# Kernel tuning notes

Measured on AMD Instinct MI355X. Metric: run time of the kernel, lower is better.

The kernel has to match this reference:

```python
import jax, jax.numpy as jnp
import numpy as np

N = 8192          # nodes
E = 131072        # edges (avg degree 16)
F_IN = 4          # in_channels
F_HID = 128       # GCNConv output channels (hard-coded in module)
C = 16            # out_channels = number of clusters
EPS = 1e-15


def setup_inputs() -> dict:
    key = jax.random.key(0)
    ks = jax.random.split(key, 6)
    x = jax.random.normal(ks[0], (N, F_IN), dtype=jnp.float32)
    W1 = jax.random.normal(ks[1], (F_IN, F_HID), dtype=jnp.float32) / np.sqrt(F_IN)
    b1 = jax.random.normal(ks[2], (F_HID,), dtype=jnp.float32) * 0.01
    Wp = jax.random.normal(ks[3], (F_HID, C), dtype=jnp.float32) / np.sqrt(F_HID)
    bp = jax.random.normal(ks[4], (C,), dtype=jnp.float32) * 0.01
    edge_index = jax.random.randint(ks[5], (2, E), 0, N, dtype=jnp.int64)
    batch = jnp.zeros((N,), dtype=jnp.int64)  # single graph
    return {"x": x, "W1": W1, "b1": b1, "Wp": Wp, "bp": bp,
            "edge_index": edge_index, "batch": batch}


def gcn_conv(x, edge_index, W, b):
    # PyG GCNConv: add self loops, symmetric D^{-1/2}(A+I)D^{-1/2} normalization.
    src, dst = edge_index[0], edge_index[1]
    h = x @ W                                      # [N, F_HID]
    ones = jnp.ones(src.shape[0], dtype=h.dtype)
    deg = jax.ops.segment_sum(ones, dst, num_segments=N) + 1.0  # +1 self loop
    dinv = jax.lax.rsqrt(deg)
    norm = dinv[src] * dinv[dst]                   # [E]
    agg = jax.ops.segment_sum(h[src] * norm[:, None], dst, num_segments=N)
    agg = agg + h * (dinv * dinv)[:, None]         # self-loop message
    return agg + b


def dmon_pool(x, adj, Wp, bp):
    # x: [1, N, F_HID], adj: [1, N, N]; mask is all-ones (single full graph)
    s = jax.nn.softmax(x @ Wp + bp, axis=-1)       # [1, N, C]
    out = jax.nn.selu(jnp.einsum('bnc,bnf->bcf', s, x))     # [1, C, F_HID]
    out_adj = jnp.einsum('bnc,bnm,bmk->bck', s, adj, s)     # [1, C, C]

    # Spectral (modularity) loss
    deg = adj.sum(axis=1)[..., None]               # column sums, [1, N, 1]
    m = deg.sum(axis=(1, 2)) / 2.0                 # [1]
    ca = jnp.einsum('bnc,bnl->bcl', s, deg)        # [1, C, 1]
    normalizer = jnp.matmul(ca, jnp.swapaxes(ca, 1, 2)) / 2.0 / m[:, None, None]
    spectral = (-jnp.trace(out_adj - normalizer, axis1=1, axis2=2) / 2.0 / m).mean()

    # Orthogonality loss
    ss = jnp.einsum('bnc,bnk->bck', s, s)          # [1, C, C]
    i_s = jnp.eye(C, dtype=s.dtype)
    ss_fro = jnp.sqrt(jnp.sum(ss * ss, axis=(1, 2), keepdims=True))
    diff = ss / ss_fro - i_s / jnp.sqrt(jnp.asarray(C, s.dtype))
    ortho = jnp.sqrt(jnp.sum(diff * diff, axis=(1, 2))).mean()

    # Cluster (collapse) loss
    cluster_size = s.sum(axis=1)                   # [1, C]
    cluster = (jnp.linalg.norm(cluster_size, axis=1) / N
               * jnp.sqrt(jnp.asarray(C, s.dtype)) - 1.0).mean()

    # Fix and normalize coarsened adjacency
    ind = jnp.arange(C)
    out_adj = out_adj.at[:, ind, ind].set(0.0)
    d = jnp.sqrt(out_adj.sum(axis=-1))[:, :, None] + EPS   # [1, C, 1]
    out_adj = out_adj / d / jnp.swapaxes(d, 1, 2)
    return s, out, out_adj, spectral, ortho, cluster


def reference(x, W1, b1, Wp, bp, edge_index, batch):
    h = jax.nn.relu(gcn_conv(x, edge_index, W1, b1))        # [N, 128]
    xd = h[None]                                            # to_dense_batch, B=1
    src, dst = edge_index[0], edge_index[1]
    adj = jnp.zeros((N, N), dtype=h.dtype).at[src, dst].add(1.0)[None]  # to_dense_adj
    s, out, out_adj, sp, o, c = dmon_pool(xd, adj, Wp, bp)
    return jax.nn.log_softmax(out, axis=-1), sp + o + c, s
```

## Files before the change

kernel.cpp:

```cpp
#include <hip/hip_runtime.h>
#include <math.h>

#define NN 8192
#define FH 128
#define NC 16
#define HP 132
#define CHUNK 32

#define WS_CNT   0
#define WS_OFF   8192
#define WS_CUR   16448
#define WS_DINV  24640
#define WS_CSRC  32832
#define WS_XD    163904
#define WS_ORAW  196672
#define WS_SS    204864
#define WS_CA    205888
#define WS_CS    206144
#define WS_TR    206400
#define WS_END   206912
#define WS_ACC_BEGIN_F4 49168
#define WS_ACC_COUNT_F4 2560

__global__ __launch_bounds__(256) void k_zero(float4* __restrict__ ws) {
    int i = blockIdx.x * blockDim.x + threadIdx.x;
    if (i < NN / 4) ws[i] = make_float4(0.f, 0.f, 0.f, 0.f);
}

__global__ __launch_bounds__(128) void k_count(const int* __restrict__ ei,
                                               float* __restrict__ ws, int E) {
    int t = threadIdx.x, b = blockIdx.x;
    if (b < 20) {
        reinterpret_cast<float4*>(ws)[WS_ACC_BEGIN_F4 + b * 128 + t] =
            make_float4(0.f, 0.f, 0.f, 0.f);
    }
    int* cnt = (int*)(ws + WS_CNT);
    int e = b * 128 + t;
    if (e < E) atomicAdd(&cnt[ei[E + e]], 1);
}

__global__ __launch_bounds__(256) void k_prefix(float* __restrict__ ws) {
    int* cnt  = (int*)(ws + WS_CNT);
    int* off  = (int*)(ws + WS_OFF);
    int* cur  = (int*)(ws + WS_CUR);
    float* dinv = ws + WS_DINV;
    __shared__ int psum[256];
    int t = threadIdx.x;
    int base = t * 32;
    int local[32];
    int sum = 0;
    #pragma unroll
    for (int k = 0; k < 32; ++k) { local[k] = cnt[base + k]; sum += local[k]; }
    psum[t] = sum;
    __syncthreads();
    for (int o = 1; o < 256; o <<= 1) {
        int v = (t >= o) ? psum[t - o] : 0;
        __syncthreads();
        psum[t] += v;
        __syncthreads();
    }
    int run = psum[t] - sum;
    #pragma unroll
    for (int k = 0; k < 32; ++k) {
        off[base + k] = run;
        cur[base + k] = run;
        dinv[base + k] = rsqrtf((float)local[k] + 1.0f);
        run += local[k];
    }
    if (t == 255) off[NN] = run;
}

__global__ __launch_bounds__(128) void k_fill(const int* __restrict__ ei,
                                              const float* __restrict__ x,
                                              float* __restrict__ ws, int E) {
    int t = threadIdx.x, b = blockIdx.x;
    if (b < 64) {
        int n = b * 128 + t;
        float di = ws[WS_DINV + n];
        float4 xv = reinterpret_cast<const float4*>(x)[n];
        reinterpret_cast<float4*>(ws + WS_XD)[n] =
            make_float4(xv.x * di, xv.y * di, xv.z * di, xv.w * di);
    }
    int* cur  = (int*)(ws + WS_CUR);
    int* csrc = (int*)(ws + WS_CSRC);
    int e = b * 128 + t;
    if (e >= E) return;
    int s = ei[e], d = ei[E + e];
    int slot = atomicAdd(&cur[d], 1);
    csrc[slot] = s;
}

__global__ __launch_bounds__(256) void k_node(const float* __restrict__ W1,
                                              const float* __restrict__ b1,
                                              const float* __restrict__ Wp,
                                              const float* __restrict__ bp,
                                              float* __restrict__ ws,
                                              float* __restrict__ s_out) {
    int*   cnti = (int*)(ws + WS_CNT);
    int*   off  = (int*)(ws + WS_OFF);
    int*   csrc = (int*)(ws + WS_CSRC);
    float* dinv = ws + WS_DINV;
    const float4* xd = reinterpret_cast<const float4*>(ws + WS_XD);
    float* oraw = ws + WS_ORAW;
    float* ssb  = ws + WS_SS;
    float* cab  = ws + WS_CA;
    float* csb  = ws + WS_CS;

    __shared__ float h_lds[CHUNK][HP];
    __shared__ float wpT[NC * HP];
    __shared__ float s_lds[CHUNK][NC];
    __shared__ float z_lds[CHUNK][4];
    __shared__ float c_lds[CHUNK];
    int t = threadIdx.x;
    int b = blockIdx.x;
    int base = b * CHUNK;

    #pragma unroll
    for (int r = 0; r < 8; ++r) {
        int idx = r * 256 + t;
        wpT[(idx & 15) * HP + (idx >> 4)] = Wp[idx];
    }

    {
        int i = t >> 3, j = t & 7;
        int o0 = off[base + i], o1 = off[base + i + 1];
        float ax = 0.f, ay = 0.f, az = 0.f, aw = 0.f;
        for (int slot = o0 + j; slot < o1; slot += 8) {
            int sN = csrc[slot];
            float4 xv = xd[sN];
            ax += xv.x; ay += xv.y; az += xv.z; aw += xv.w;
        }
        #pragma unroll
        for (int o = 4; o; o >>= 1) {
            ax += __shfl_down(ax, o, 8);
            ay += __shfl_down(ay, o, 8);
            az += __shfl_down(az, o, 8);
            aw += __shfl_down(aw, o, 8);
        }
        if (j == 0) {
            float cn = (float)cnti[base + i];
            c_lds[i] = cn;
            float dn = dinv[base + i];
            float4 xv = xd[base + i];
            z_lds[i][0] = dn * (ax + xv.x);
            z_lds[i][1] = dn * (ay + xv.y);
            z_lds[i][2] = dn * (az + xv.z);
            z_lds[i][3] = dn * (aw + xv.w);
        }
    }
    __syncthreads();

    int f = t & 127;
    {
        float w0 = W1[f], w1 = W1[128 + f], w2 = W1[256 + f], w3 = W1[384 + f];
        float bb = b1[f];
        int n0 = t >> 7;
        #pragma unroll
        for (int r = 0; r < 16; ++r) {
            int n = n0 + r * 2;
            float v = fmaf(z_lds[n][0], w0, bb);
            v = fmaf(z_lds[n][1], w1, v);
            v = fmaf(z_lds[n][2], w2, v);
            v = fmaf(z_lds[n][3], w3, v);
            h_lds[n][f] = fmaxf(v, 0.0f);
        }
    }
    __syncthreads();

    int c = t & 15, g = t >> 4;
    const float4* wrow = reinterpret_cast<const float4*>(&wpT[c * HP]);
    #pragma unroll
    for (int pass = 0; pass < 2; ++pass) {
        int n = pass * 16 + g;
        const float4* hrow = reinterpret_cast<const float4*>(&h_lds[n][0]);
        float logit = bp[c];
        #pragma unroll 8
        for (int q = 0; q < 32; ++q) {
            float4 hv = hrow[q];
            float4 wv = wrow[q];
            logit = fmaf(hv.x, wv.x, logit);
            logit = fmaf(hv.y, wv.y, logit);
            logit = fmaf(hv.z, wv.z, logit);
            logit = fmaf(hv.w, wv.w, logit);
        }
        float m = logit;
        #pragma unroll
        for (int o = 8; o; o >>= 1) m = fmaxf(m, __shfl_xor(m, o, 16));
        float ex = expf(logit - m);
        float sum = ex;
        #pragma unroll
        for (int o = 8; o; o >>= 1) sum += __shfl_xor(sum, o, 16);
        float sv = ex / sum;
        s_lds[n][c] = sv;
        s_out[(base + n) * NC + c] = sv;
    }
    __syncthreads();

    float acc[8] = {0, 0, 0, 0, 0, 0, 0, 0};
    float acc_ss = 0.0f, acc_ca = 0.0f, acc_cs = 0.0f;
    int ch = t >> 7;
    int cS = t >> 4, kS = t & 15;
    #pragma unroll
    for (int i = 0; i < CHUNK; ++i) {
        float hv = h_lds[i][f];
        const float4* sv = reinterpret_cast<const float4*>(&s_lds[i][0]);
        float4 sa = sv[ch * 2], sb = sv[ch * 2 + 1];
        acc[0] = fmaf(sa.x, hv, acc[0]);
        acc[1] = fmaf(sa.y, hv, acc[1]);
        acc[2] = fmaf(sa.z, hv, acc[2]);
        acc[3] = fmaf(sa.w, hv, acc[3]);
        acc[4] = fmaf(sb.x, hv, acc[4]);
        acc[5] = fmaf(sb.y, hv, acc[5]);
        acc[6] = fmaf(sb.z, hv, acc[6]);
        acc[7] = fmaf(sb.w, hv, acc[7]);
        acc_ss = fmaf(s_lds[i][cS], s_lds[i][kS], acc_ss);
    }
    if (t < NC) {
        #pragma unroll
        for (int i = 0; i < CHUNK; ++i) {
            acc_ca = fmaf(s_lds[i][t], c_lds[i], acc_ca);
            acc_cs += s_lds[i][t];
        }
    }
    int rep = b & 3;
    #pragma unroll
    for (int j = 0; j < 8; ++j)
        atomicAdd(&oraw[rep * 2048 + (ch * 8 + j) * FH + f], acc[j]);
    atomicAdd(&ssb[rep * 256 + cS * NC + kS], acc_ss);
    if (t < NC) {
        int rep16 = b & 15;
        atomicAdd(&cab[rep16 * NC + t], acc_ca);
        atomicAdd(&csb[rep16 * NC + t], acc_cs);
    }
}

__global__ __launch_bounds__(256) void k_adj(const int* __restrict__ ei,
                                             const float* __restrict__ s,
                                             float* __restrict__ ws, int E) {
    float* trb = ws + WS_TR;

    int t = threadIdx.x;
    int b = blockIdx.x;
    int e = b * 256 + t;

    float acc = 0.0f;
    if (e < E) {
        int sN = ei[e], dN = ei[E + e];
        const float4* sr = reinterpret_cast<const float4*>(&s[sN * NC]);
        const float4* dr = reinterpret_cast<const float4*>(&s[dN * NC]);
        float4 a0 = sr[0], a1 = sr[1], a2 = sr[2], a3 = sr[3];
        float4 b0 = dr[0], b1 = dr[1], b2 = dr[2], b3 = dr[3];
        acc = a0.x * b0.x + a0.y * b0.y + a0.z * b0.z + a0.w * b0.w;
        acc = fmaf(a1.x, b1.x, acc); acc = fmaf(a1.y, b1.y, acc);
        acc = fmaf(a1.z, b1.z, acc); acc = fmaf(a1.w, b1.w, acc);
        acc = fmaf(a2.x, b2.x, acc); acc = fmaf(a2.y, b2.y, acc);
        acc = fmaf(a2.z, b2.z, acc); acc = fmaf(a2.w, b2.w, acc);
        acc = fmaf(a3.x, b3.x, acc); acc = fmaf(a3.y, b3.y, acc);
        acc = fmaf(a3.z, b3.z, acc); acc = fmaf(a3.w, b3.w, acc);
    }
    #pragma unroll
    for (int o = 32; o; o >>= 1) acc += __shfl_xor(acc, o, 64);
    if ((t & 63) == 0) {
        int wave = (b * 256 + t) >> 6;
        atomicAdd(&trb[(wave & 15) * 32], acc);
    }
}

__device__ __forceinline__ float selu_f(float x) {
    const float a = 1.6732632423543772f, sc = 1.0507009873554805f;
    return sc * (x > 0.0f ? x : a * (expf(x) - 1.0f));
}

__global__ __launch_bounds__(256) void k_final(float* __restrict__ ws,
                                               float* __restrict__ d_out, float Ef) {
    float* oraw = ws + WS_ORAW;
    float* ssb  = ws + WS_SS;
    float* cab  = ws + WS_CA;
    float* csb  = ws + WS_CS;
    float* trb  = ws + WS_TR;
    int t = threadIdx.x;
    int lane = t & 63, w = t >> 6;

    if (w == 0) {
        float tot[4];
        float fr2 = 0.f;
        #pragma unroll
        for (int j = 0; j < 4; ++j) {
            int i = lane + j * 64;
            float v = ssb[i] + ssb[256 + i] + ssb[512 + i] + ssb[768 + i];
            tot[j] = v;
            fr2 += v * v;
        }
        #pragma unroll
        for (int o = 32; o; o >>= 1) fr2 += __shfl_xor(fr2, o, 64);
        float fro = sqrtf(fr2);
        float o2 = 0.f;
        #pragma unroll
        for (int j = 0; j < 4; ++j) {
            int i = lane + j * 64;
            float d = tot[j] / fro - ((i % 17 == 0) ? 0.25f : 0.f);
            o2 += d * d;
        }
        #pragma unroll
        for (int o = 32; o; o >>= 1) o2 += __shfl_xor(o2, o, 64);
        float ortho = sqrtf(o2);

        float tv = 0.f, ca = 0.f, cs = 0.f;
        if (lane < 16) {
            tv = trb[lane * 32];
            #pragma unroll
            for (int r = 0; r < 16; ++r) { ca += cab[r * 16 + lane]; cs += csb[r * 16 + lane]; }
        }
        float tr = tv, can = ca * ca, csn = cs * cs;
        #pragma unroll
        for (int o = 32; o; o >>= 1) {
            tr  += __shfl_xor(tr, o, 64);
            can += __shfl_xor(can, o, 64);
            csn += __shfl_xor(csn, o, 64);
        }
        float spectral = -(tr - can / Ef) / Ef;
        float cluster = sqrtf(csn) / (float)NN * 4.0f - 1.0f;
        if (lane == 0) d_out[NC * FH] = spectral + ortho + cluster;
    }

    #pragma unroll
    for (int rr = 0; rr < 4; ++rr) {
        int cR = w + rr * 4;
        int c0 = lane * 2;
        float va = 0.f, vb = 0.f;
        #pragma unroll
        for (int r = 0; r < 4; ++r) {
            float2 vv = *reinterpret_cast<const float2*>(&oraw[r * 2048 + cR * FH + c0]);
            va += vv.x;
            vb += vv.y;
        }
        va = selu_f(va);
        vb = selu_f(vb);
        float mx = fmaxf(va, vb);
        #pragma unroll
        for (int o = 32; o; o >>= 1) mx = fmaxf(mx, __shfl_xor(mx, o, 64));
        float sm = expf(va - mx) + expf(vb - mx);
        #pragma unroll
        for (int o = 32; o; o >>= 1) sm += __shfl_xor(sm, o, 64);
        float ls = mx + logf(sm);
        d_out[cR * FH + c0]     = va - ls;
        d_out[cR * FH + c0 + 1] = vb - ls;
    }
}

extern "C" void kernel_launch(void* const* d_in, const int* in_sizes, int n_in,
                              void* d_out, int out_size, void* d_ws, size_t ws_size,
                              hipStream_t stream) {
    const float* x  = (const float*)d_in[0];
    const float* W1 = (const float*)d_in[1];
    const float* b1 = (const float*)d_in[2];
    const float* Wp = (const float*)d_in[3];
    const float* bp = (const float*)d_in[4];
    const int*   ei = (const int*)d_in[5];
    int E = in_sizes[5] / 2;

    float* ws  = (float*)d_ws;
    float* out = (float*)d_out;
    float* s   = out + NC * FH + 1;

    k_zero  <<<8, 256, 0, stream>>>((float4*)d_ws);
    k_count <<<(E + 127) / 128, 128, 0, stream>>>(ei, ws, E);
    k_prefix<<<1, 256, 0, stream>>>(ws);
    k_fill  <<<(E + 127) / 128, 128, 0, stream>>>(ei, x, ws, E);
    k_node  <<<NN / CHUNK, 256, 0, stream>>>(W1, b1, Wp, bp, ws, s);
    k_adj   <<<(E + 255) / 256, 256, 0, stream>>>(ei, s, ws, E);
    k_final <<<1, 256, 0, stream>>>(ws, out, (float)E);
}
```

Before: 54.20 us.

## Replace contended float atomics in k_node with per-block partials reduced in k_adj

Each k_node block now writes its oraw and ss partial sums to its own slab instead of doing atomicAdds into 4 replicated copies. Nine extra blocks appended to the k_adj launch reduce the 256 slabs into final buffers, which k_final reads directly. This removes heavy atomic contention (256 blocks by 2048 addresses) at the cost of roughly 2 MB of extra workspace traffic and a serial 256-step reduction loop in a few blocks that overlaps the edge-trace work.

New measurement: 63.79 us. 17.7% more time.

```diff
diff --git a/kernel.cpp b/kernel.cpp
--- a/kernel.cpp
+++ b/kernel.cpp
@@ -13,14 +13,16 @@
 #define WS_DINV  24640
 #define WS_CSRC  32832
 #define WS_XD    163904
-#define WS_ORAW  196672
-#define WS_SS    204864
-#define WS_CA    205888
-#define WS_CS    206144
-#define WS_TR    206400
-#define WS_END   206912
-#define WS_ACC_BEGIN_F4 49168
-#define WS_ACC_COUNT_F4 2560
+#define WS_ORAWS 196672
+#define WS_SSS   720960
+#define WS_ORAWF 786496
+#define WS_SSF   788544
+#define WS_CA    788800
+#define WS_CS    789056
+#define WS_TR    789312
+#define WS_END   789824
+#define WS_ZACC_F4 197200
+#define WS_ZACC_N  256
 
 __global__ __launch_bounds__(256) void k_zero(float4* __restrict__ ws) {
     int i = blockIdx.x * blockDim.x + threadIdx.x;
@@ -30,9 +32,9 @@
 __global__ __launch_bounds__(128) void k_count(const int* __restrict__ ei,
                                                float* __restrict__ ws, int E) {
     int t = threadIdx.x, b = blockIdx.x;
-    if (b < 20) {
-        reinterpret_cast<float4*>(ws)[WS_ACC_BEGIN_F4 + b * 128 + t] =
-            make_float4(0.f, 0.f, 0.f, 0.f);
+    if (b == 0) {
+        reinterpret_cast<float4*>(ws)[WS_ZACC_F4 + t] = make_float4(0.f, 0.f, 0.f, 0.f);
+        reinterpret_cast<float4*>(ws)[WS_ZACC_F4 + 128 + t] = make_float4(0.f, 0.f, 0.f, 0.f);
     }
     int* cnt = (int*)(ws + WS_CNT);
     int e = b * 128 + t;
@@ -101,10 +103,10 @@
     int*   csrc = (int*)(ws + WS_CSRC);
     float* dinv = ws + WS_DINV;
     const float4* xd = reinterpret_cast<const float4*>(ws + WS_XD);
-    float* oraw = ws + WS_ORAW;
-    float* ssb  = ws + WS_SS;
-    float* cab  = ws + WS_CA;
-    float* csb  = ws + WS_CS;
+    float* oraws = ws + WS_ORAWS;
+    float* sss   = ws + WS_SSS;
+    float* cab   = ws + WS_CA;
+    float* csb   = ws + WS_CS;
 
     __shared__ float h_lds[CHUNK][HP];
     __shared__ float wpT[NC * HP];
@@ -222,11 +224,10 @@
             acc_cs += s_lds[i][t];
         }
     }
-    int rep = b & 3;
     #pragma unroll
     for (int j = 0; j < 8; ++j)
-        atomicAdd(&oraw[rep * 2048 + (ch * 8 + j) * FH + f], acc[j]);
-    atomicAdd(&ssb[rep * 256 + cS * NC + kS], acc_ss);
+        oraws[b * 2048 + (ch * 8 + j) * FH + f] = acc[j];
+    sss[b * 256 + t] = acc_ss;
     if (t < NC) {
         int rep16 = b & 15;
         atomicAdd(&cab[rep16 * NC + t], acc_ca);
@@ -236,33 +237,47 @@
 
 __global__ __launch_bounds__(256) void k_adj(const int* __restrict__ ei,
                                              const float* __restrict__ s,
-                                             float* __restrict__ ws, int E) {
-    float* trb = ws + WS_TR;
-
+                                             float* __restrict__ ws, int E, int tb) {
     int t = threadIdx.x;
     int b = blockIdx.x;
-    int e = b * 256 + t;
-
-    float acc = 0.0f;
-    if (e < E) {
-        int sN = ei[e], dN = ei[E + e];
-        const float4* sr = reinterpret_cast<const float4*>(&s[sN * NC]);
-        const float4* dr = reinterpret_cast<const float4*>(&s[dN * NC]);
-        float4 a0 = sr[0], a1 = sr[1], a2 = sr[2], a3 = sr[3];
-        float4 b0 = dr[0], b1 = dr[1], b2 = dr[2], b3 = dr[3];
-        acc = a0.x * b0.x + a0.y * b0.y + a0.z * b0.z + a0.w * b0.w;
-        acc = fmaf(a1.x, b1.x, acc); acc = fmaf(a1.y, b1.y, acc);
-        acc = fmaf(a1.z, b1.z, acc); acc = fmaf(a1.w, b1.w, acc);
-        acc = fmaf(a2.x, b2.x, acc); acc = fmaf(a2.y, b2.y, acc);
-        acc = fmaf(a2.z, b2.z, acc); acc = fmaf(a2.w, b2.w, acc);
-        acc = fmaf(a3.x, b3.x, acc); acc = fmaf(a3.y, b3.y, acc);
-        acc = fmaf(a3.z, b3.z, acc); acc = fmaf(a3.w, b3.w, acc);
-    }
-    #pragma unroll
-    for (int o = 32; o; o >>= 1) acc += __shfl_xor(acc, o, 64);
-    if ((t & 63) == 0) {
-        int wave = (b * 256 + t) >> 6;
-        atomicAdd(&trb[(wave & 15) * 32], acc);
+
+    if (b < tb) {
+        float* trb = ws + WS_TR;
+        int e = b * 256 + t;
+        float acc = 0.0f;
+        if (e < E) {
+            int sN = ei[e], dN = ei[E + e];
+            const float4* sr = reinterpret_cast<const float4*>(&s[sN * NC]);
+            const float4* dr = reinterpret_cast<const float4*>(&s[dN * NC]);
+            float4 a0 = sr[0], a1 = sr[1], a2 = sr[2], a3 = sr[3];
+            float4 b0 = dr[0], b1 = dr[1], b2 = dr[2], b3 = dr[3];
+            acc = a0.x * b0.x + a0.y * b0.y + a0.z * b0.z + a0.w * b0.w;
+            acc = fmaf(a1.x, b1.x, acc); acc = fmaf(a1.y, b1.y, acc);
+            acc = fmaf(a1.z, b1.z, acc); acc = fmaf(a1.w, b1.w, acc);
+            acc = fmaf(a2.x, b2.x, acc); acc = fmaf(a2.y, b2.y, acc);
+            acc = fmaf(a2.z, b2.z, acc); acc = fmaf(a2.w, b2.w, acc);
+            acc = fmaf(a3.x, b3.x, acc); acc = fmaf(a3.y, b3.y, acc);
+            acc = fmaf(a3.z, b3.z, acc); acc = fmaf(a3.w, b3.w, acc);
+        }
+        #pragma unroll
+        for (int o = 32; o; o >>= 1) acc += __shfl_xor(acc, o, 64);
+        if ((t & 63) == 0) {
+            int wave = (b * 256 + t) >> 6;
+            atomicAdd(&trb[(wave & 15) * 32], acc);
+        }
+    } else if (b < tb + 8) {
+        const float* slab = ws + WS_ORAWS;
+        int col = (b - tb) * 256 + t;
+        float v = 0.f;
+        #pragma unroll 8
+        for (int p = 0; p < 256; ++p) v += slab[p * 2048 + col];
+        ws[WS_ORAWF + col] = v;
+    } else {
+        const float* slab = ws + WS_SSS;
+        float v = 0.f;
+        #pragma unroll 8
+        for (int p = 0; p < 256; ++p) v += slab[p * 256 + t];
+        ws[WS_SSF + t] = v;
     }
 }
 
@@ -273,11 +288,11 @@
 
 __global__ __launch_bounds__(256) void k_final(float* __restrict__ ws,
                                                float* __restrict__ d_out, float Ef) {
-    float* oraw = ws + WS_ORAW;
-    float* ssb  = ws + WS_SS;
-    float* cab  = ws + WS_CA;
-    float* csb  = ws + WS_CS;
-    float* trb  = ws + WS_TR;
+    float* orawf = ws + WS_ORAWF;
+    float* ssf   = ws + WS_SSF;
+    float* cab   = ws + WS_CA;
+    float* csb   = ws + WS_CS;
+    float* trb   = ws + WS_TR;
     int t = threadIdx.x;
     int lane = t & 63, w = t >> 6;
 
@@ -287,7 +302,7 @@
         #pragma unroll
         for (int j = 0; j < 4; ++j) {
             int i = lane + j * 64;
-            float v = ssb[i] + ssb[256 + i] + ssb[512 + i] + ssb[768 + i];
+            float v = ssf[i];
             tot[j] = v;
             fr2 += v * v;
         }
@@ -327,15 +342,9 @@
     for (int rr = 0; rr < 4; ++rr) {
         int cR = w + rr * 4;
         int c0 = lane * 2;
-        float va = 0.f, vb = 0.f;
-        #pragma unroll
-        for (int r = 0; r < 4; ++r) {
-            float2 vv = *reinterpret_cast<const float2*>(&oraw[r * 2048 + cR * FH + c0]);
-            va += vv.x;
-            vb += vv.y;
-        }
-        va = selu_f(va);
-        vb = selu_f(vb);
+        float2 vv = *reinterpret_cast<const float2*>(&orawf[cR * FH + c0]);
+        float va = selu_f(vv.x);
+        float vb = selu_f(vv.y);
         float mx = fmaxf(va, vb);
         #pragma unroll
         for (int o = 32; o; o >>= 1) mx = fmaxf(mx, __shfl_xor(mx, o, 64));
@@ -363,11 +372,13 @@
     float* out = (float*)d_out;
     float* s   = out + NC * FH + 1;
 
+    int tb = (E + 255) / 256;
+
     k_zero  <<<8, 256, 0, stream>>>((float4*)d_ws);
     k_count <<<(E + 127) / 128, 128, 0, stream>>>(ei, ws, E);
     k_prefix<<<1, 256, 0, stream>>>(ws);
     k_fill  <<<(E + 127) / 128, 128, 0, stream>>>(ei, x, ws, E);
     k_node  <<<NN / CHUNK, 256, 0, stream>>>(W1, b1, Wp, bp, ws, s);
-    k_adj   <<<(E + 255) / 256, 256, 0, stream>>>(ei, s, ws, E);
+    k_adj   <<<tb + 9, 256, 0, stream>>>(ei, s, ws, E, tb);
     k_final <<<1, 256, 0, stream>>>(ws, out, (float)E);
 }
```
